# Optimization experiments

Measured on AMD Instinct MI355X. Metric: run time of the kernel, lower is better.

The kernel has to match this reference:

```python
import jax, jax.numpy as jnp
import numpy as np
from itertools import product

# dims
V, B, C, H, Wd = 3, 4, 64, 120, 160   # views, batch, feat2d_channel, image H/W
D3 = 96                               # feat3d_dim
G = 64                                # voxel grid side
N = 200000                            # sparse voxel count
NL = 250000                           # number of link rows
K = 27                                # 3^3 sparse-conv kernel offsets
EPS = 1e-5


def _build_kernel_map(rng):
    # unique sparse coordinates (b,x,y,z) sampled from a B*G^3 grid, sorted by linear code
    lin = np.sort(rng.choice(B * G * G * G, size=N, replace=False)).astype(np.int64)
    b = lin // (G * G * G)
    r = lin % (G * G * G)
    x = r // (G * G)
    y = (r // G) % G
    z = r % G
    in_idx = np.zeros((K, N), np.int32)
    mask = np.zeros((K, N), bool)
    for k, (dx, dy, dz) in enumerate(product((-1, 0, 1), repeat=3)):
        qx, qy, qz = x + dx, y + dy, z + dz
        inb = (qx >= 0) & (qx < G) & (qy >= 0) & (qy < G) & (qz >= 0) & (qz < G)
        qc = ((b * G + np.clip(qx, 0, G - 1)) * G + np.clip(qy, 0, G - 1)) * G + np.clip(qz, 0, G - 1)
        pos = np.clip(np.searchsorted(lin, qc), 0, N - 1)
        ok = inb & (lin[pos] == qc)
        in_idx[k] = np.where(ok, pos, 0)
        mask[k] = ok
    return jnp.asarray(in_idx), jnp.asarray(mask)


def setup_inputs() -> dict:
    rng = np.random.default_rng(0)
    key = jax.random.key(0)
    ks = jax.random.split(key, 8)
    feat_2d_all = jax.random.normal(ks[0], (V, B, C, H, Wd), jnp.float32)
    feat3d_F = jax.random.normal(ks[1], (N, D3), jnp.float32)
    # links: (NL, 4, V) = [batch_idx, v(row), u(col), valid]
    links = np.stack([
        rng.integers(0, B, (NL, V)),
        rng.integers(0, H, (NL, V)),
        rng.integers(0, Wd, (NL, V)),
        rng.integers(0, 2, (NL, V)),
    ], axis=1).astype(np.int32)
    coords_map_out = rng.permutation(N).astype(np.int32)
    coords_map_in = rng.choice(NL, N, replace=False).astype(np.int32)
    in_idx, nbr_mask = _build_kernel_map(rng)
    s = 0.05
    W1 = jax.random.normal(ks[2], (K, V * C, C), jnp.float32) * s
    W2 = jax.random.normal(ks[3], (K, C, D3), jnp.float32) * s
    W3 = jax.random.normal(ks[4], (K, 2 * D3, D3), jnp.float32) * s
    return {
        'feat_2d_all': feat_2d_all, 'feat3d_F': feat3d_F,
        'links': jnp.asarray(links),
        'coords_map_in': jnp.asarray(coords_map_in),
        'coords_map_out': jnp.asarray(coords_map_out),
        'in_idx': in_idx, 'nbr_mask': nbr_mask,
        'W1': W1, 'g1': jnp.ones((C,)), 'b1': jnp.zeros((C,)),
        'W2': W2, 'g2': jnp.ones((D3,)), 'b2': jnp.zeros((D3,)),
        'W3': W3, 'g3': jnp.ones((D3,)), 'b3': jnp.zeros((D3,)),
    }


def _sconv(x, Wk, in_idx, nbr_mask):
    # sparse 3x3x3 conv: out[i] = sum_k x[nbr(i,k)] @ Wk[k], masked where no neighbor
    out = jnp.zeros((x.shape[0], Wk.shape[-1]), x.dtype)
    for k in range(Wk.shape[0]):
        g = x[in_idx[k]] * nbr_mask[k][:, None].astype(x.dtype)
        out = out + g @ Wk[k]
    return out


def _bn_relu(x, g, b):
    mu = x.mean(axis=0)
    var = x.var(axis=0)
    return jax.nn.relu(g * (x - mu) / jnp.sqrt(var + EPS) + b)


def reference(feat_2d_all, feat3d_F, links, coords_map_in, coords_map_out,
              in_idx, nbr_mask, W1, g1, b1, W2, g2, b2, W3, g3, b3):
    n = feat3d_F.shape[0]
    v_, c = feat_2d_all.shape[0], feat_2d_all.shape[2]
    # current_links[coords_map_out] = links[coords_map_in]
    cur = jnp.zeros((n, 4, v_), links.dtype).at[coords_map_out].set(links[coords_map_in])
    bi = cur[:, 0, :].T   # (V, n)
    hi = cur[:, 1, :].T
    wi = cur[:, 2, :].T
    val = cur[:, 3, :].T
    vs = jnp.arange(v_)[:, None]
    # per-view gather from (V,B,C,H,W): advanced indices around the channel slice -> (V, n, C)
    g = feat_2d_all[vs, bi, :, hi, wi]
    g = g * val[:, :, None].astype(g.dtype)
    feat_2d_to_3d = jnp.transpose(g, (1, 0, 2)).reshape(n, v_ * c)
    # view_fusion: conv3 -> BN -> ReLU -> conv3 -> BN -> ReLU
    h = _bn_relu(_sconv(feat_2d_to_3d, W1, in_idx, nbr_mask), g1, b1)
    h = _bn_relu(_sconv(h, W2, in_idx, nbr_mask), g2, b2)
    # cat with 3d features, fuse_to_3d: conv3 -> BN -> ReLU
    cat = jnp.concatenate([feat3d_F, h], axis=-1)
    out = _bn_relu(_sconv(cat, W3, in_idx, nbr_mask), g3, b3)
    return out
```

## Files before the change

### kernel.cpp

```cpp
#include <hip/hip_runtime.h>
#include <stdint.h>


constexpr int NPT = 200000;
constexpr int KNB = 27;

typedef unsigned short u16;
typedef __attribute__((ext_vector_type(8))) short     bf16x8;
typedef __attribute__((ext_vector_type(8))) unsigned short u16x8;
typedef __attribute__((ext_vector_type(4))) float     f32x4;

static __device__ __forceinline__ u16 f2bf(float f){
  unsigned int u = __float_as_uint(f);
  unsigned int r = (u + 0x7fffu + ((u >> 16) & 1u)) >> 16;
  return (u16)r;
}
static __device__ __forceinline__ float bf2f(u16 u){
  return __uint_as_float(((unsigned int)u) << 16);
}

static __device__ __forceinline__ void gload_lds16(const void* g, void* l){
  __builtin_amdgcn_global_load_lds(
      (const __attribute__((address_space(1))) void*)g,
      (__attribute__((address_space(3))) void*)(uint32_t)(uintptr_t)l,
      16, 0, 0);
}

__global__ void detect_mask_kernel(const int* __restrict__ m32, int* __restrict__ flag){
  if (threadIdx.x == 0 && blockIdx.x == 0){
    int ok = 1;
    for (int i = 0; i < 64; ++i){ int v = m32[i]; if (v != 0 && v != 1) ok = 0; }
    *flag = ok ? 2 : 0;
  }
}

__global__ __launch_bounds__(256) void transpose2d_kernel(const float* __restrict__ in,
                                                          u16* __restrict__ out){
  __shared__ float tile[64][33];
  int bid = blockIdx.x;
  int wt = bid % 5;  int rest = bid / 5;
  int h  = rest % 120; rest /= 120;
  int b  = rest % 4;  int v = rest / 4;
  int w0 = wt * 32;
  int tx = threadIdx.x & 31;
  int ty = threadIdx.x >> 5;
  const float* ip = in + ((size_t)(v*4 + b) * 64) * 19200 + h * 160 + w0;
  #pragma unroll
  for (int cc = 0; cc < 8; ++cc){
    int c = cc * 8 + ty;
    tile[c][tx] = ip[(size_t)c * 19200 + tx];
  }
  __syncthreads();
  u16* op = out + (((size_t)(v*4 + b) * 120 + h) * 160 + w0) * 64;
  int c = threadIdx.x & 63;
  int wg = threadIdx.x >> 6;
  #pragma unroll
  for (int i = 0; i < 8; ++i){
    int w = wg + i * 4;
    op[(size_t)w * 64 + c] = f2bf(tile[c][w]);
  }
}

__global__ void wconvert_kernel(const float* __restrict__ src, u16* __restrict__ dst,
                                int cin, int cout){
  int gid = blockIdx.x * 256 + threadIdx.x;
  int tot = KNB * cin * cout;
  if (gid >= tot) return;
  int ncb = cout / 16;
  int nkc = cin / 32;
  int e    = gid & 7;
  int lane = (gid >> 3) & 63;
  int f    = gid >> 9;
  int cb   = f % ncb;  f /= ncb;
  int kc   = f % nkc;
  int k    = f / nkc;
  int ci = kc * 32 + (lane >> 4) * 8 + e;
  int co = cb * 16 + (lane & 15);
  dst[gid] = f2bf(src[((size_t)k * cin + ci) * cout + co]);
}

__global__ void stage_a_kernel(const u16* __restrict__ ft, const int* __restrict__ links,
                               const int* __restrict__ cmi, const int* __restrict__ cmo,
                               u16* __restrict__ x0){
  int gid = blockIdx.x * 256 + threadIdx.x;
  if (gid >= NPT * 3) return;
  int i = gid / 3;
  int v = gid - i * 3;
  int outr = cmo[i];
  int l    = cmi[i];
  int b  = links[l*12 + v];
  int h  = links[l*12 + 3 + v];
  int w  = links[l*12 + 6 + v];
  int vl = links[l*12 + 9 + v];
  u16* dst = x0 + (size_t)outr * 192 + v * 64;
  if (vl){
    const u16* src = ft + (((size_t)(v*4 + b) * 120 + h) * 160 + w) * 64;
    #pragma unroll
    for (int j = 0; j < 8; ++j) ((u16x8*)dst)[j] = ((const u16x8*)src)[j];
  } else {
    u16x8 z = {};
    #pragma unroll
    for (int j = 0; j < 8; ++j) ((u16x8*)dst)[j] = z;
  }
}

__global__ void f3convert_kernel(const float* __restrict__ src, u16* __restrict__ dst){
  long gid = (long)blockIdx.x * 256 + threadIdx.x;
  long tot8 = (long)NPT * 12;
  if (gid >= tot8) return;
  int row = (int)(gid / 12);
  int c0  = (int)(gid % 12) * 8;
  const float* s = src + (size_t)row * 96 + c0;
  u16* d = dst + (size_t)row * 192 + c0;
  #pragma unroll
  for (int j = 0; j < 8; ++j) d[j] = f2bf(s[j]);
}

template<int CIN, int COUT, bool F32OUT>
__global__ __launch_bounds__(256)
void conv_kernel(const u16* __restrict__ x0, const u16* __restrict__ wt,
                 const int* __restrict__ in_idx,
                 const uint8_t* __restrict__ mbytes,
                 const int* __restrict__ flagp, void* __restrict__ outp,
                 int outStride, float* __restrict__ st){
  constexpr int NCB    = COUT / 16;
  constexpr int NKC    = CIN / 32;
  constexpr int WELE   = CIN * COUT;
  constexpr int ROUNDS = (WELE * 2) / 4096;
  __shared__ __align__(16) u16 wlds[2 * WELE];
  __shared__ float shS[COUT], shQ[COUT];

  const int tid    = threadIdx.x;
  const int lane   = tid & 63;
  const int wv     = tid >> 6;
  const int r16    = lane & 15;
  const int kgrp   = lane >> 4;
  const int m0     = blockIdx.x * 128;
  const int mshift = *flagp;

  if (tid < COUT){ shS[tid] = 0.f; shQ[tid] = 0.f; }

  f32x4 acc[2][NCB];
  #pragma unroll
  for (int rt = 0; rt < 2; ++rt)
    #pragma unroll
    for (int cb = 0; cb < NCB; ++cb) acc[rt][cb] = (f32x4)0.0f;

  int rowc[2];
  #pragma unroll
  for (int rt = 0; rt < 2; ++rt){
    int row = m0 + wv * 32 + rt * 16 + r16;
    rowc[rt] = row < NPT ? row : NPT - 1;
  }

  #pragma unroll
  for (int rd = 0; rd < ROUNDS; ++rd){
    int chunk = rd * 4 + wv;
    gload_lds16((const char*)wt + chunk * 1024 + lane * 16,
                (char*)wlds + chunk * 1024);
  }
  int idC[2]; bool mC[2];
  #pragma unroll
  for (int rt = 0; rt < 2; ++rt){
    idC[rt] = in_idx[rowc[rt]];
    mC[rt]  = mbytes[(size_t)rowc[rt] << mshift] != 0;
  }
  __syncthreads();

  const u16* xk = x0 + kgrp * 8;

  for (int k = 0; k < KNB; ++k){
    if (k + 1 < KNB){
      const u16* wn = wt + (size_t)(k + 1) * WELE;
      char* wd = (char*)wlds + ((k + 1) & 1) * (WELE * 2);
      #pragma unroll
      for (int rd = 0; rd < ROUNDS; ++rd){
        int chunk = rd * 4 + wv;
        gload_lds16((const char*)wn + chunk * 1024 + lane * 16,
                    wd + chunk * 1024);
      }
    }

    bf16x8 a0[NKC], a1[NKC];
    #pragma unroll
    for (int kc = 0; kc < NKC; ++kc){ bf16x8 z = {}; a0[kc] = z; a1[kc] = z; }
    if (mC[0]){
      const u16* b0 = xk + (size_t)idC[0] * CIN;
      #pragma unroll
      for (int kc = 0; kc < NKC; ++kc) a0[kc] = *(const bf16x8*)(b0 + kc * 32);
    }
    if (mC[1]){
      const u16* b1 = xk + (size_t)idC[1] * CIN;
      #pragma unroll
      for (int kc = 0; kc < NKC; ++kc) a1[kc] = *(const bf16x8*)(b1 + kc * 32);
    }

    if (k + 1 < KNB){
      #pragma unroll
      for (int rt = 0; rt < 2; ++rt){
        size_t o = (size_t)(k + 1) * NPT + rowc[rt];
        idC[rt] = in_idx[o];
        mC[rt]  = mbytes[o << mshift] != 0;
      }
    }

    const u16* wb = &wlds[(k & 1) * WELE];
    #pragma unroll
    for (int kc = 0; kc < NKC; ++kc){
      #pragma unroll
      for (int cb = 0; cb < NCB; ++cb){
        bf16x8 b = *(const bf16x8*)&wb[((kc * NCB + cb) * 64 + lane) * 8];
        acc[0][cb] = __builtin_amdgcn_mfma_f32_16x16x32_bf16(a0[kc], b, acc[0][cb], 0, 0, 0);
        acc[1][cb] = __builtin_amdgcn_mfma_f32_16x16x32_bf16(a1[kc], b, acc[1][cb], 0, 0, 0);
      }
    }
    __syncthreads();
  }

  #pragma unroll
  for (int rt = 0; rt < 2; ++rt){
    #pragma unroll
    for (int cb = 0; cb < NCB; ++cb){
      const int cout = cb * 16 + r16;
      float s = 0.f, q = 0.f;
      #pragma unroll
      for (int j = 0; j < 4; ++j){
        int row = m0 + wv * 32 + rt * 16 + kgrp * 4 + j;
        if (row < NPT){
          float v = acc[rt][cb][j];
          if (F32OUT) ((float*)outp)[(size_t)row * outStride + cout] = v;
          else        ((u16*)outp)[(size_t)row * outStride + cout] = f2bf(v);
          s += v; q += v * v;
        }
      }
      atomicAdd(&shS[cout], s); atomicAdd(&shQ[cout], q);
    }
  }
  __syncthreads();
  if (tid < COUT){
    atomicAdd(&st[tid],        shS[tid]);
    atomicAdd(&st[COUT + tid], shQ[tid]);
  }
}

template<int CCH, bool ISF32>
__global__ void bnrelu_kernel(void* __restrict__ xp, int stride,
                              const float* __restrict__ st,
                              const float* __restrict__ gg, const float* __restrict__ bb){
  const float invN = 1.0f / (float)NPT;
  constexpr int GPR = CCH / 8;
  long tot8 = (long)NPT * GPR;
  for (long e8 = (long)blockIdx.x * 256 + threadIdx.x; e8 < tot8; e8 += (long)gridDim.x * 256){
    int row = (int)(e8 / GPR);
    int c0  = (int)(e8 % GPR) * 8;
    size_t base = (size_t)row * stride + c0;
    #pragma unroll
    for (int j = 0; j < 8; ++j){
      int c = c0 + j;
      float mu  = st[c] * invN;
      float var = st[CCH + c] * invN - mu * mu;
      float rs  = rsqrtf(var + 1e-5f);
      float x;
      if (ISF32) x = ((float*)xp)[base + j];
      else       x = bf2f(((u16*)xp)[base + j]);
      float y = gg[c] * (x - mu) * rs + bb[c];
      y = y > 0.f ? y : 0.f;
      if (ISF32) ((float*)xp)[base + j] = y;
      else       ((u16*)xp)[base + j] = f2bf(y);
    }
  }
}

extern "C" void kernel_launch(void* const* d_in, const int* in_sizes, int n_in,
                              void* d_out, int out_size, void* d_ws, size_t ws_size,
                              hipStream_t stream){
  const float* feat2d = (const float*)d_in[0];
  const float* feat3d = (const float*)d_in[1];
  const int*   links  = (const int*)d_in[2];
  const int*   cmi    = (const int*)d_in[3];
  const int*   cmo    = (const int*)d_in[4];
  const int*   inidx  = (const int*)d_in[5];
  const void*  mask   = d_in[6];
  const float* W1 = (const float*)d_in[7];
  const float* g1 = (const float*)d_in[8];
  const float* b1 = (const float*)d_in[9];
  const float* W2 = (const float*)d_in[10];
  const float* g2 = (const float*)d_in[11];
  const float* b2 = (const float*)d_in[12];
  const float* W3 = (const float*)d_in[13];
  const float* g3 = (const float*)d_in[14];
  const float* b3 = (const float*)d_in[15];

  char* ws = (char*)d_ws;
  u16* X0 = (u16*)(ws + 0);
  constexpr size_t OFF_B  = 76800512;
  u16* FT = (u16*)(ws + OFF_B);
  u16* Z1 = (u16*)(ws + OFF_B);
  u16* WT1 = (u16*)(ws + 106291712);
  u16* WT2 = WT1 + 27 * 192 * 64;
  u16* WT3 = WT2 + 27 * 64 * 96;
  float* ST  = (float*)(ws + 108282368);
  float* ST1 = ST;
  float* ST2 = ST + 128;
  float* ST3 = ST + 320;
  int*   FLAG = (int*)(ST + 512);

  hipMemsetAsync(ST, 0, 513 * sizeof(float), stream);
  detect_mask_kernel<<<1, 64, 0, stream>>>((const int*)mask, FLAG);
  transpose2d_kernel<<<7200, 256, 0, stream>>>(feat2d, FT);
  wconvert_kernel<<<(27*192*64 + 255)/256, 256, 0, stream>>>(W1, WT1, 192, 64);
  wconvert_kernel<<<(27*64*96  + 255)/256, 256, 0, stream>>>(W2, WT2, 64, 96);
  wconvert_kernel<<<(27*192*96 + 255)/256, 256, 0, stream>>>(W3, WT3, 192, 96);
  stage_a_kernel<<<(NPT*3 + 255)/256, 256, 0, stream>>>(FT, links, cmi, cmo, X0);

  const int nblk = (NPT + 127) / 128;
  const uint8_t* m8 = (const uint8_t*)mask;

  conv_kernel<192, 64, false><<<nblk, 256, 0, stream>>>(X0, WT1, inidx, m8, FLAG, Z1, 64, ST1);
  bnrelu_kernel<64, false><<<2048, 256, 0, stream>>>(Z1, 64, ST1, g1, b1);

  f3convert_kernel<<<((NPT*12) + 255)/256, 256, 0, stream>>>(feat3d, X0);

  conv_kernel<64, 96, false><<<nblk, 256, 0, stream>>>(Z1, WT2, inidx, m8, FLAG, X0 + 96, 192, ST2);
  bnrelu_kernel<96, false><<<2048, 256, 0, stream>>>(X0 + 96, 192, ST2, g2, b2);

  conv_kernel<192, 96, true><<<nblk, 256, 0, stream>>>(X0, WT3, inidx, m8, FLAG, d_out, 96, ST3);
  bnrelu_kernel<96, true><<<2048, 256, 0, stream>>>(d_out, 96, ST3, g3, b3);
}
```

Before: 859.8 us.

## Split conv1 and conv3 output channels across two blocks per row tile

```diff
diff --git a/kernel.cpp b/kernel.cpp
--- a/kernel.cpp
+++ b/kernel.cpp
@@ -62,11 +62,11 @@
 }
 
 __global__ void wconvert_kernel(const float* __restrict__ src, u16* __restrict__ dst,
-                                int cin, int cout){
+                                int cin, int coutT, int coutF, int cbase){
   int gid = blockIdx.x * 256 + threadIdx.x;
-  int tot = KNB * cin * cout;
+  int tot = KNB * cin * coutT;
   if (gid >= tot) return;
-  int ncb = cout / 16;
+  int ncb = coutT / 16;
   int nkc = cin / 32;
   int e    = gid & 7;
   int lane = (gid >> 3) & 63;
@@ -75,8 +75,8 @@
   int kc   = f % nkc;
   int k    = f / nkc;
   int ci = kc * 32 + (lane >> 4) * 8 + e;
-  int co = cb * 16 + (lane & 15);
-  dst[gid] = f2bf(src[((size_t)k * cin + ci) * cout + co]);
+  int co = cbase + cb * 16 + (lane & 15);
+  dst[gid] = f2bf(src[((size_t)k * cin + ci) * coutF + co]);
 }
 
 __global__ void stage_a_kernel(const u16* __restrict__ ft, const int* __restrict__ links,
@@ -116,29 +116,36 @@
   for (int j = 0; j < 8; ++j) d[j] = f2bf(s[j]);
 }
 
-template<int CIN, int COUT, bool F32OUT>
+template<int CIN, int COUT_T, bool COLSPLIT, bool F32OUT>
 __global__ __launch_bounds__(256)
-void conv_kernel(const u16* __restrict__ x0, const u16* __restrict__ wt,
+void conv_kernel(const u16* __restrict__ x0,
+                 const u16* __restrict__ wtA, const u16* __restrict__ wtB,
                  const int* __restrict__ in_idx,
                  const uint8_t* __restrict__ mbytes,
                  const int* __restrict__ flagp, void* __restrict__ outp,
                  int outStride, float* __restrict__ st){
-  constexpr int NCB    = COUT / 16;
+  constexpr int NCB    = COUT_T / 16;
   constexpr int NKC    = CIN / 32;
-  constexpr int WELE   = CIN * COUT;
-  constexpr int ROUNDS = (WELE * 2) / 4096;
+  constexpr int WELE   = CIN * COUT_T;
+  constexpr int NCHUNK = (WELE * 2) / 1024;
+  constexpr int ROUNDS = (NCHUNK + 3) / 4;
+  constexpr int COUTF  = COLSPLIT ? COUT_T * 2 : COUT_T;
   __shared__ __align__(16) u16 wlds[2 * WELE];
-  __shared__ float shS[COUT], shQ[COUT];
+  __shared__ float shS[COUT_T], shQ[COUT_T];
 
   const int tid    = threadIdx.x;
   const int lane   = tid & 63;
   const int wv     = tid >> 6;
   const int r16    = lane & 15;
   const int kgrp   = lane >> 4;
-  const int m0     = blockIdx.x * 128;
+  const int bid    = blockIdx.x;
+  const int half   = COLSPLIT ? (bid & 1) : 0;
+  const int m0     = (COLSPLIT ? (bid >> 1) : bid) * 128;
+  const int cbase  = half * COUT_T;
+  const u16* wt    = (COLSPLIT && half) ? wtB : wtA;
   const int mshift = *flagp;
 
-  if (tid < COUT){ shS[tid] = 0.f; shQ[tid] = 0.f; }
+  if (tid < COUT_T){ shS[tid] = 0.f; shQ[tid] = 0.f; }
 
   f32x4 acc[2][NCB];
   #pragma unroll
@@ -156,8 +163,9 @@
   #pragma unroll
   for (int rd = 0; rd < ROUNDS; ++rd){
     int chunk = rd * 4 + wv;
-    gload_lds16((const char*)wt + chunk * 1024 + lane * 16,
-                (char*)wlds + chunk * 1024);
+    if (chunk < NCHUNK)
+      gload_lds16((const char*)wt + chunk * 1024 + lane * 16,
+                  (char*)wlds + chunk * 1024);
   }
   int idC[2]; bool mC[2];
   #pragma unroll
@@ -176,8 +184,9 @@
       #pragma unroll
       for (int rd = 0; rd < ROUNDS; ++rd){
         int chunk = rd * 4 + wv;
-        gload_lds16((const char*)wn + chunk * 1024 + lane * 16,
-                    wd + chunk * 1024);
+        if (chunk < NCHUNK)
+          gload_lds16((const char*)wn + chunk * 1024 + lane * 16,
+                      wd + chunk * 1024);
       }
     }
 
@@ -228,8 +237,8 @@
         int row = m0 + wv * 32 + rt * 16 + kgrp * 4 + j;
         if (row < NPT){
           float v = acc[rt][cb][j];
-          if (F32OUT) ((float*)outp)[(size_t)row * outStride + cout] = v;
-          else        ((u16*)outp)[(size_t)row * outStride + cout] = f2bf(v);
+          if (F32OUT) ((float*)outp)[(size_t)row * outStride + cbase + cout] = v;
+          else        ((u16*)outp)[(size_t)row * outStride + cbase + cout] = f2bf(v);
           s += v; q += v * v;
         }
       }
@@ -237,9 +246,9 @@
     }
   }
   __syncthreads();
-  if (tid < COUT){
-    atomicAdd(&st[tid],        shS[tid]);
-    atomicAdd(&st[COUT + tid], shQ[tid]);
+  if (tid < COUT_T){
+    atomicAdd(&st[cbase + tid],         shS[tid]);
+    atomicAdd(&st[COUTF + cbase + tid], shQ[tid]);
   }
 }
 
@@ -296,9 +305,11 @@
   constexpr size_t OFF_B  = 76800512;
   u16* FT = (u16*)(ws + OFF_B);
   u16* Z1 = (u16*)(ws + OFF_B);
-  u16* WT1 = (u16*)(ws + 106291712);
-  u16* WT2 = WT1 + 27 * 192 * 64;
-  u16* WT3 = WT2 + 27 * 64 * 96;
+  u16* WT1a = (u16*)(ws + 106291712);
+  u16* WT1b = WT1a + 27 * 192 * 32;
+  u16* WT2  = WT1b + 27 * 192 * 32;
+  u16* WT3a = WT2  + 27 * 64 * 96;
+  u16* WT3b = WT3a + 27 * 192 * 48;
   float* ST  = (float*)(ws + 108282368);
   float* ST1 = ST;
   float* ST2 = ST + 128;
@@ -308,22 +319,27 @@
   hipMemsetAsync(ST, 0, 513 * sizeof(float), stream);
   detect_mask_kernel<<<1, 64, 0, stream>>>((const int*)mask, FLAG);
   transpose2d_kernel<<<7200, 256, 0, stream>>>(feat2d, FT);
-  wconvert_kernel<<<(27*192*64 + 255)/256, 256, 0, stream>>>(W1, WT1, 192, 64);
-  wconvert_kernel<<<(27*64*96  + 255)/256, 256, 0, stream>>>(W2, WT2, 64, 96);
-  wconvert_kernel<<<(27*192*96 + 255)/256, 256, 0, stream>>>(W3, WT3, 192, 96);
+  wconvert_kernel<<<(27*192*32 + 255)/256, 256, 0, stream>>>(W1, WT1a, 192, 32, 64, 0);
+  wconvert_kernel<<<(27*192*32 + 255)/256, 256, 0, stream>>>(W1, WT1b, 192, 32, 64, 32);
+  wconvert_kernel<<<(27*64*96  + 255)/256, 256, 0, stream>>>(W2, WT2, 64, 96, 96, 0);
+  wconvert_kernel<<<(27*192*48 + 255)/256, 256, 0, stream>>>(W3, WT3a, 192, 48, 96, 0);
+  wconvert_kernel<<<(27*192*48 + 255)/256, 256, 0, stream>>>(W3, WT3b, 192, 48, 96, 48);
   stage_a_kernel<<<(NPT*3 + 255)/256, 256, 0, stream>>>(FT, links, cmi, cmo, X0);
 
   const int nblk = (NPT + 127) / 128;
   const uint8_t* m8 = (const uint8_t*)mask;
 
-  conv_kernel<192, 64, false><<<nblk, 256, 0, stream>>>(X0, WT1, inidx, m8, FLAG, Z1, 64, ST1);
+  conv_kernel<192, 32, true, false><<<2 * nblk, 256, 0, stream>>>(
+      X0, WT1a, WT1b, inidx, m8, FLAG, Z1, 64, ST1);
   bnrelu_kernel<64, false><<<2048, 256, 0, stream>>>(Z1, 64, ST1, g1, b1);
 
   f3convert_kernel<<<((NPT*12) + 255)/256, 256, 0, stream>>>(feat3d, X0);
 
-  conv_kernel<64, 96, false><<<nblk, 256, 0, stream>>>(Z1, WT2, inidx, m8, FLAG, X0 + 96, 192, ST2);
+  conv_kernel<64, 96, false, false><<<nblk, 256, 0, stream>>>(
+      Z1, WT2, nullptr, inidx, m8, FLAG, X0 + 96, 192, ST2);
   bnrelu_kernel<96, false><<<2048, 256, 0, stream>>>(X0 + 96, 192, ST2, g2, b2);
 
-  conv_kernel<192, 96, true><<<nblk, 256, 0, stream>>>(X0, WT3, inidx, m8, FLAG, d_out, 96, ST3);
+  conv_kernel<192, 48, true, true><<<2 * nblk, 256, 0, stream>>>(
+      X0, WT3a, WT3b, inidx, m8, FLAG, d_out, 96, ST3);
   bnrelu_kernel<96, true><<<2048, 256, 0, stream>>>(d_out, 96, ST3, g3, b3);
 }
```

After: 899.0 us. 4.6% more time.

## Single-buffer conv weights, branchless zero-row gather, XCD-aware block remap

Applied to the files above, without the earlier changes.

```diff
diff --git a/kernel.cpp b/kernel.cpp
--- a/kernel.cpp
+++ b/kernel.cpp
@@ -122,20 +122,24 @@
                  const int* __restrict__ in_idx,
                  const uint8_t* __restrict__ mbytes,
                  const int* __restrict__ flagp, void* __restrict__ outp,
-                 int outStride, float* __restrict__ st){
+                 int outStride, float* __restrict__ st, int nwork){
   constexpr int NCB    = COUT / 16;
   constexpr int NKC    = CIN / 32;
   constexpr int WELE   = CIN * COUT;
-  constexpr int ROUNDS = (WELE * 2) / 4096;
-  __shared__ __align__(16) u16 wlds[2 * WELE];
+  constexpr int NCHUNK = (WELE * 2) / 1024;
+  constexpr int ROUNDS = (NCHUNK + 3) / 4;
+  __shared__ __align__(16) u16 wlds[WELE];
   __shared__ float shS[COUT], shQ[COUT];
+
+  const int v = (blockIdx.x & 7) * (gridDim.x >> 3) + (blockIdx.x >> 3);
+  if (v >= nwork) return;
 
   const int tid    = threadIdx.x;
   const int lane   = tid & 63;
   const int wv     = tid >> 6;
   const int r16    = lane & 15;
   const int kgrp   = lane >> 4;
-  const int m0     = blockIdx.x * 128;
+  const int m0     = v * 128;
   const int mshift = *flagp;
 
   if (tid < COUT){ shS[tid] = 0.f; shQ[tid] = 0.f; }
@@ -156,65 +160,59 @@
   #pragma unroll
   for (int rd = 0; rd < ROUNDS; ++rd){
     int chunk = rd * 4 + wv;
-    gload_lds16((const char*)wt + chunk * 1024 + lane * 16,
-                (char*)wlds + chunk * 1024);
-  }
-  int idC[2]; bool mC[2];
+    if (chunk < NCHUNK)
+      gload_lds16((const char*)wt + chunk * 1024 + lane * 16,
+                  (char*)wlds + chunk * 1024);
+  }
+  int vC[2];
   #pragma unroll
   for (int rt = 0; rt < 2; ++rt){
-    idC[rt] = in_idx[rowc[rt]];
-    mC[rt]  = mbytes[(size_t)rowc[rt] << mshift] != 0;
+    int id = in_idx[rowc[rt]];
+    int mv = mbytes[(size_t)rowc[rt] << mshift];
+    vC[rt] = mv ? id : NPT;
   }
   __syncthreads();
 
   const u16* xk = x0 + kgrp * 8;
 
   for (int k = 0; k < KNB; ++k){
-    if (k + 1 < KNB){
-      const u16* wn = wt + (size_t)(k + 1) * WELE;
-      char* wd = (char*)wlds + ((k + 1) & 1) * (WELE * 2);
-      #pragma unroll
-      for (int rd = 0; rd < ROUNDS; ++rd){
-        int chunk = rd * 4 + wv;
-        gload_lds16((const char*)wn + chunk * 1024 + lane * 16,
-                    wd + chunk * 1024);
-      }
-    }
-
-    bf16x8 a0[NKC], a1[NKC];
-    #pragma unroll
-    for (int kc = 0; kc < NKC; ++kc){ bf16x8 z = {}; a0[kc] = z; a1[kc] = z; }
-    if (mC[0]){
-      const u16* b0 = xk + (size_t)idC[0] * CIN;
-      #pragma unroll
-      for (int kc = 0; kc < NKC; ++kc) a0[kc] = *(const bf16x8*)(b0 + kc * 32);
-    }
-    if (mC[1]){
-      const u16* b1 = xk + (size_t)idC[1] * CIN;
-      #pragma unroll
-      for (int kc = 0; kc < NKC; ++kc) a1[kc] = *(const bf16x8*)(b1 + kc * 32);
-    }
+    const u16* gb0 = xk + (size_t)vC[0] * CIN;
+    const u16* gb1 = xk + (size_t)vC[1] * CIN;
 
     if (k + 1 < KNB){
       #pragma unroll
       for (int rt = 0; rt < 2; ++rt){
         size_t o = (size_t)(k + 1) * NPT + rowc[rt];
-        idC[rt] = in_idx[o];
-        mC[rt]  = mbytes[o << mshift] != 0;
+        int id = in_idx[o];
+        int mv = mbytes[o << mshift];
+        vC[rt] = mv ? id : NPT;
       }
     }
 
-    const u16* wb = &wlds[(k & 1) * WELE];
     #pragma unroll
     for (int kc = 0; kc < NKC; ++kc){
+      bf16x8 a0 = *(const bf16x8*)(gb0 + kc * 32);
+      bf16x8 a1 = *(const bf16x8*)(gb1 + kc * 32);
       #pragma unroll
       for (int cb = 0; cb < NCB; ++cb){
-        bf16x8 b = *(const bf16x8*)&wb[((kc * NCB + cb) * 64 + lane) * 8];
-        acc[0][cb] = __builtin_amdgcn_mfma_f32_16x16x32_bf16(a0[kc], b, acc[0][cb], 0, 0, 0);
-        acc[1][cb] = __builtin_amdgcn_mfma_f32_16x16x32_bf16(a1[kc], b, acc[1][cb], 0, 0, 0);
+        bf16x8 b = *(const bf16x8*)&wlds[((kc * NCB + cb) * 64 + lane) * 8];
+        acc[0][cb] = __builtin_amdgcn_mfma_f32_16x16x32_bf16(a0, b, acc[0][cb], 0, 0, 0);
+        acc[1][cb] = __builtin_amdgcn_mfma_f32_16x16x32_bf16(a1, b, acc[1][cb], 0, 0, 0);
       }
     }
     __syncthreads();
+
+    if (k + 1 < KNB){
+      const u16* wn = wt + (size_t)(k + 1) * WELE;
+      #pragma unroll
+      for (int rd = 0; rd < ROUNDS; ++rd){
+        int chunk = rd * 4 + wv;
+        if (chunk < NCHUNK)
+          gload_lds16((const char*)wn + chunk * 1024 + lane * 16,
+                      (char*)wlds + chunk * 1024);
+      }
+      __syncthreads();
+    }
   }
 
   #pragma unroll
@@ -227,10 +225,10 @@
       for (int j = 0; j < 4; ++j){
         int row = m0 + wv * 32 + rt * 16 + kgrp * 4 + j;
         if (row < NPT){
-          float v = acc[rt][cb][j];
-          if (F32OUT) ((float*)outp)[(size_t)row * outStride + cout] = v;
-          else        ((u16*)outp)[(size_t)row * outStride + cout] = f2bf(v);
-          s += v; q += v * v;
+          float v2 = acc[rt][cb][j];
+          if (F32OUT) ((float*)outp)[(size_t)row * outStride + cout] = v2;
+          else        ((u16*)outp)[(size_t)row * outStride + cout] = f2bf(v2);
+          s += v2; q += v2 * v2;
         }
       }
       atomicAdd(&shS[cout], s); atomicAdd(&shQ[cout], q);
@@ -313,17 +311,24 @@
   wconvert_kernel<<<(27*192*96 + 255)/256, 256, 0, stream>>>(W3, WT3, 192, 96);
   stage_a_kernel<<<(NPT*3 + 255)/256, 256, 0, stream>>>(FT, links, cmi, cmo, X0);
 
+  hipMemsetAsync(ws + (size_t)NPT * 384, 0, 384, stream);
+  hipMemsetAsync(ws + OFF_B + (size_t)NPT * 128, 0, 128, stream);
+
   const int nblk = (NPT + 127) / 128;
+  const int grid = ((nblk + 7) / 8) * 8;
   const uint8_t* m8 = (const uint8_t*)mask;
 
-  conv_kernel<192, 64, false><<<nblk, 256, 0, stream>>>(X0, WT1, inidx, m8, FLAG, Z1, 64, ST1);
+  conv_kernel<192, 64, false><<<grid, 256, 0, stream>>>(
+      X0, WT1, inidx, m8, FLAG, Z1, 64, ST1, nblk);
   bnrelu_kernel<64, false><<<2048, 256, 0, stream>>>(Z1, 64, ST1, g1, b1);
 
   f3convert_kernel<<<((NPT*12) + 255)/256, 256, 0, stream>>>(feat3d, X0);
 
-  conv_kernel<64, 96, false><<<nblk, 256, 0, stream>>>(Z1, WT2, inidx, m8, FLAG, X0 + 96, 192, ST2);
+  conv_kernel<64, 96, false><<<grid, 256, 0, stream>>>(
+      Z1, WT2, inidx, m8, FLAG, X0 + 96, 192, ST2, nblk);
   bnrelu_kernel<96, false><<<2048, 256, 0, stream>>>(X0 + 96, 192, ST2, g2, b2);
 
-  conv_kernel<192, 96, true><<<nblk, 256, 0, stream>>>(X0, WT3, inidx, m8, FLAG, d_out, 96, ST3);
+  conv_kernel<192, 96, true><<<grid, 256, 0, stream>>>(
+      X0, WT3, inidx, m8, FLAG, d_out, 96, ST3, nblk);
   bnrelu_kernel<96, true><<<2048, 256, 0, stream>>>(d_out, 96, ST3, g3, b3);
 }
```

Measured after the change: 816.4 us. -5.1%, faster.
